# Performance work log

Measured on AMD Instinct MI355X. Metric: run time of the kernel, lower is better.

Reference implementation:

```python
import jax, jax.numpy as jnp
import numpy as np


def setup_inputs() -> dict:
    key = jax.random.key(0)
    k = jax.random.split(key, 5)
    B, Cin, Cout, H, W = 16, 32, 32, 256, 256
    m1, m2 = 16, 16
    scale = (1.0 / (Cin * Cout)) ** 0.5  # RandomUniform limit in original
    x = jax.random.normal(k[0], (B, Cin, H, W), dtype=jnp.float32)
    ws = {
        'w1_real': jax.random.uniform(k[1], (Cin, Cout, m1, m2), jnp.float32, -scale, scale),
        'w1_imag': jax.random.uniform(k[2], (Cin, Cout, m1, m2), jnp.float32, -scale, scale),
        'w2_real': jax.random.uniform(k[3], (Cin, Cout, m1, m2), jnp.float32, -scale, scale),
        'w2_imag': jax.random.uniform(k[4], (Cin, Cout, m1, m2), jnp.float32, -scale, scale),
    }
    return {'x': x, **ws}


def reference(x, w1_real, w1_imag, w2_real, w2_imag):
    B, Cin, H, W = x.shape
    Cout, m1, m2 = w1_real.shape[1], w1_real.shape[2], w1_real.shape[3]
    Wr = W // 2 + 1
    # full rFFT2 over (H, W); x_ft: [B, Cin, H, Wr] complex64
    x_ft = jnp.fft.rfft2(x, axes=(-2, -1))
    w1 = w1_real + 1j * w1_imag  # [Cin, Cout, m1, m2]
    w2 = w2_real + 1j * w2_imag
    top = jnp.einsum('bixy,ioxy->boxy', x_ft[:, :, :m1, :m2], w1)
    bottom = jnp.einsum('bixy,ioxy->boxy', x_ft[:, :, -m1:, :m2], w2)
    out_ft = jnp.zeros((B, Cout, H, Wr), dtype=x_ft.dtype)
    out_ft = out_ft.at[:, :, :m1, :m2].set(top)
    # original pads bottom block to start at row h_ft - m1 and ADDS the two padded tensors
    out_ft = out_ft.at[:, :, H - m1:, :m2].add(bottom)
    return jnp.fft.irfft2(out_ft, s=(H, W), axes=(-2, -1))
```

## Files before the change

### kernel.cpp

```cpp
#include <hip/hip_runtime.h>
#include <math.h>


#define TWO_PI_256 0.0245436926f

typedef short short8 __attribute__((ext_vector_type(8)));
typedef float f32x4  __attribute__((ext_vector_type(4)));

__device__ __forceinline__ ushort f2bf(float v) {
    unsigned u = __float_as_uint(v);
    u += 0x7FFFu + ((u >> 16) & 1u);
    return (ushort)(u >> 16);
}
__device__ __forceinline__ float bf2f(ushort h) {
    return __uint_as_float(((unsigned)h) << 16);
}

__global__ void init_frags(ushort* __restrict__ Fr) {
    const int s = blockIdx.x;
    const int lane = threadIdx.x;
    const int q = lane >> 4, n = lane & 15;
    for (int j = 0; j < 8; ++j) {
        float v = 0.f;
        int hl;
        if (s < 32) {
            int tn = s >> 4; hl = (s >> 3) & 1; int ch = s & 7;
            int w = ch * 32 + q * 8 + j, ky = n;
            float sn, cs; __sincosf((float)((w * ky) & 255) * TWO_PI_256, &sn, &cs);
            v = tn == 0 ? cs : -sn;
        } else if (s < 160) {
            int s2 = s - 32; int mt = s2 >> 5; hl = (s2 >> 4) & 1; int ch = s2 & 15;
            int m = mt * 16 + n, k = ch * 32 + q * 8 + j;
            int kxi = m >> 1, rx = m & 1, h = k >> 1, rt = k & 1;
            int r = kxi + (kxi >= 16 ? 224 : 0);
            float sn, cs; __sincosf((float)((r * h) & 255) * TWO_PI_256, &sn, &cs);
            v = (rx == 0) ? (rt == 0 ? cs : sn) : (rt == 0 ? -sn : cs);
        } else if (s < 288) {
            int s3 = s - 160; int mtG = s3 >> 2; hl = (s3 >> 1) & 1; int ch = s3 & 1;
            int m = mtG * 16 + n, k = ch * 32 + q * 8 + j;
            int h = m >> 1, rg = m & 1, kxi = k >> 1, ry = k & 1;
            int r = kxi + (kxi >= 16 ? 224 : 0);
            float sn, cs; __sincosf((float)((r * h) & 255) * TWO_PI_256, &sn, &cs);
            v = ((rg == 0) ? (ry == 0 ? cs : -sn) : (ry == 0 ? sn : cs)) * (1.0f / 65536.0f);
        } else {
            int s4 = s - 288; int nt = s4 >> 1; hl = s4 & 1;
            int k = q * 8 + j, w = nt * 16 + n;
            int ky = k >> 1, ri = k & 1;
            float sn, cs; __sincosf((float)((w * ky) & 255) * TWO_PI_256, &sn, &cs);
            v = (ky == 0) ? (ri ? 0.f : 1.f) : (ri ? -2.f * sn : 2.f * cs);
        }
        ushort hi = f2bf(v);
        Fr[s * 512 + lane * 8 + j] = hl == 0 ? hi : f2bf(v - bf2f(hi));
    }
}

__global__ __launch_bounds__(512) void f12_gemm(const float* __restrict__ x,
                                                const ushort* __restrict__ Fr,
                                                float* __restrict__ X) {
    __shared__ ushort LDS[16384];
    ushort* Ah = LDS;
    ushort* Al = LDS + 8192;
    ushort* Ts = LDS;

    const int t = threadIdx.x, bi = blockIdx.x;
    const int lane = t & 63, w = t >> 6;
    const int q = lane >> 4, n = lane & 15;
    const int srow = t >> 3, sw4 = t & 7;
    const float* xb = x + (size_t)bi * 65536;

    f32x4 acc[2][2];
    #pragma unroll
    for (int a = 0; a < 2; ++a)
        #pragma unroll
        for (int bb = 0; bb < 2; ++bb) acc[a][bb] = (f32x4){0.f, 0.f, 0.f, 0.f};

    for (int ch = 0; ch < 8; ++ch) {
        __syncthreads();
        #pragma unroll
        for (int m = 0; m < 4; ++m) {
            const int row = srow + 64 * m;
            float4 v = *(const float4*)(xb + (size_t)row * 256 + ch * 32 + sw4 * 4);
            ushort h0_ = f2bf(v.x), h1 = f2bf(v.y), h2 = f2bf(v.z), h3 = f2bf(v.w);
            *(ushort4*)&Ah[row * 32 + sw4 * 4] = make_ushort4(h0_, h1, h2, h3);
            *(ushort4*)&Al[row * 32 + sw4 * 4] = make_ushort4(f2bf(v.x - bf2f(h0_)), f2bf(v.y - bf2f(h1)),
                                                              f2bf(v.z - bf2f(h2)), f2bf(v.w - bf2f(h3)));
        }
        __syncthreads();

        short8 bh0 = *(const short8*)&Fr[(size_t)(0  + ch) * 512 + lane * 8];
        short8 bl0 = *(const short8*)&Fr[(size_t)(8  + ch) * 512 + lane * 8];
        short8 bh1 = *(const short8*)&Fr[(size_t)(16 + ch) * 512 + lane * 8];
        short8 bl1 = *(const short8*)&Fr[(size_t)(24 + ch) * 512 + lane * 8];

        #pragma unroll
        for (int mt = 0; mt < 2; ++mt) {
            const int row = w * 32 + mt * 16 + n;
            short8 ah = *(const short8*)&Ah[row * 32 + q * 8];
            short8 al = *(const short8*)&Al[row * 32 + q * 8];
            acc[mt][0] = __builtin_amdgcn_mfma_f32_16x16x32_bf16(al, bh0, acc[mt][0], 0, 0, 0);
            acc[mt][0] = __builtin_amdgcn_mfma_f32_16x16x32_bf16(ah, bl0, acc[mt][0], 0, 0, 0);
            acc[mt][0] = __builtin_amdgcn_mfma_f32_16x16x32_bf16(ah, bh0, acc[mt][0], 0, 0, 0);
            acc[mt][1] = __builtin_amdgcn_mfma_f32_16x16x32_bf16(al, bh1, acc[mt][1], 0, 0, 0);
            acc[mt][1] = __builtin_amdgcn_mfma_f32_16x16x32_bf16(ah, bl1, acc[mt][1], 0, 0, 0);
            acc[mt][1] = __builtin_amdgcn_mfma_f32_16x16x32_bf16(ah, bh1, acc[mt][1], 0, 0, 0);
        }
    }

    __syncthreads();
    #pragma unroll
    for (int mt = 0; mt < 2; ++mt) {
        ushort h8[8], l8[8];
        #pragma unroll
        for (int j = 0; j < 8; ++j) {
            float v = acc[mt][j & 1][j >> 1];
            h8[j] = f2bf(v);
            l8[j] = f2bf(v - bf2f(h8[j]));
        }
        const int c = w * 2 + mt;
        *(short8*)&Ts[c * 1024 + lane * 8]       = *(short8*)h8;
        *(short8*)&Ts[c * 1024 + 512 + lane * 8] = *(short8*)l8;
    }
    __syncthreads();

    if (w < 4) {
        const int mt2 = w;
        f32x4 a2 = (f32x4){0.f, 0.f, 0.f, 0.f};
        #pragma unroll
        for (int c2 = 0; c2 < 16; ++c2) {
            short8 bh = *(const short8*)&Ts[c2 * 1024 + lane * 8];
            short8 bl = *(const short8*)&Ts[c2 * 1024 + 512 + lane * 8];
            short8 ah = *(const short8*)&Fr[(size_t)(32 + mt2 * 32 + c2) * 512 + lane * 8];
            short8 al = *(const short8*)&Fr[(size_t)(32 + mt2 * 32 + 16 + c2) * 512 + lane * 8];
            a2 = __builtin_amdgcn_mfma_f32_16x16x32_bf16(al, bh, a2, 0, 0, 0);
            a2 = __builtin_amdgcn_mfma_f32_16x16x32_bf16(ah, bl, a2, 0, 0, 0);
            a2 = __builtin_amdgcn_mfma_f32_16x16x32_bf16(ah, bh, a2, 0, 0, 0);
        }
        #pragma unroll
        for (int r = 0; r < 4; ++r)
            X[(size_t)(mt2 * 16 + q * 4 + r) * 8192 + bi * 16 + n] = a2[r];
    }
}

__global__ __launch_bounds__(256) void mix(const float* __restrict__ X,
                                           const float* __restrict__ w1r_, const float* __restrict__ w1i_,
                                           const float* __restrict__ w2r_, const float* __restrict__ w2i_,
                                           float* __restrict__ Y) {
    int gid = blockIdx.x * 256 + threadIdx.x;
    int ky = gid & 15, kxi = (gid >> 4) & 31, o = (gid >> 9) & 31, b = gid >> 14;
    const float* wr = (kxi < 16) ? w1r_ : w2r_;
    const float* wi = (kxi < 16) ? w1i_ : w2i_;
    int xx = kxi & 15;
    const float* Xr = X + (size_t)(kxi * 2) * 8192 + b * 512 + ky;
    const float* Xi = Xr + 8192;
    const float* wrp = wr + (size_t)(o * 16 + xx) * 16 + ky;
    const float* wip = wi + (size_t)(o * 16 + xx) * 16 + ky;
    float yr = 0.f, yi = 0.f;
    #pragma unroll 8
    for (int i = 0; i < 32; ++i) {
        float xr = Xr[i * 16], xim = Xi[i * 16];
        float wre = wrp[(size_t)i * 8192], wim = wip[(size_t)i * 8192];
        yr = fmaf(xr, wre, fmaf(-xim, wim, yr));
        yi = fmaf(xr, wim, fmaf( xim, wre, yi));
    }
    size_t yb = (size_t)(kxi * 2) * 8192 + b * 512 + o * 16 + ky;
    Y[yb] = yr;
    Y[yb + 8192] = yi;
}

__global__ __launch_bounds__(512) void i12_gemm(const float* __restrict__ Yb,
                                                const ushort* __restrict__ Fr,
                                                float* __restrict__ out) {
    __shared__ ushort Bs[2048];
    __shared__ ushort As[16384];
    const int t = threadIdx.x, bo = blockIdx.x;
    const int lane = t & 63, w = t >> 6;
    const int q = lane >> 4, n = lane & 15;
    const int b = bo >> 5, o = bo & 31;

    if (t < 256) {
        const int k = t >> 2, e4 = t & 3;
        float4 v = *(const float4*)&Yb[(size_t)k * 8192 + b * 512 + o * 16 + e4 * 4];
        const int c = k >> 5, q2 = (k >> 3) & 3, j2 = k & 7;
        float vv[4] = {v.x, v.y, v.z, v.w};
        #pragma unroll
        for (int ee = 0; ee < 4; ++ee) {
            const int ky = e4 * 4 + ee;
            ushort hi = f2bf(vv[ee]);
            Bs[c * 1024 + (q2 * 16 + ky) * 8 + j2]       = hi;
            Bs[c * 1024 + 512 + (q2 * 16 + ky) * 8 + j2] = f2bf(vv[ee] - bf2f(hi));
        }
    }
    __syncthreads();

    f32x4 g[4];
    #pragma unroll
    for (int mi = 0; mi < 4; ++mi) g[mi] = (f32x4){0.f, 0.f, 0.f, 0.f};
    #pragma unroll
    for (int ch = 0; ch < 2; ++ch) {
        short8 bh = *(const short8*)&Bs[ch * 1024 + lane * 8];
        short8 bl = *(const short8*)&Bs[ch * 1024 + 512 + lane * 8];
        #pragma unroll
        for (int mi = 0; mi < 4; ++mi) {
            const int mtG = w * 4 + mi;
            short8 ah = *(const short8*)&Fr[(size_t)(160 + mtG * 4 + ch) * 512 + lane * 8];
            short8 al = *(const short8*)&Fr[(size_t)(160 + mtG * 4 + 2 + ch) * 512 + lane * 8];
            g[mi] = __builtin_amdgcn_mfma_f32_16x16x32_bf16(al, bh, g[mi], 0, 0, 0);
            g[mi] = __builtin_amdgcn_mfma_f32_16x16x32_bf16(ah, bl, g[mi], 0, 0, 0);
            g[mi] = __builtin_amdgcn_mfma_f32_16x16x32_bf16(ah, bh, g[mi], 0, 0, 0);
        }
    }

    #pragma unroll
    for (int mi = 0; mi < 4; ++mi)
        #pragma unroll
        for (int r = 0; r < 4; ++r) {
            const int m1 = (w * 4 + mi) * 16 + q * 4 + r;
            const int h = m1 >> 1, ri = m1 & 1;
            const int k2 = 2 * n + ri;
            const int ht = h >> 4, hr = h & 15;
            const int ad = ((k2 >> 3) * 16 + hr) * 8 + (k2 & 7);
            const float v = g[mi][r];
            const ushort hi = f2bf(v);
            As[ht * 1024 + ad]       = hi;
            As[ht * 1024 + 512 + ad] = f2bf(v - bf2f(hi));
        }
    __syncthreads();

    #pragma unroll
    for (int mi2 = 0; mi2 < 2; ++mi2) {
        const int ht2 = w * 2 + mi2;
        short8 ah = *(const short8*)&As[ht2 * 1024 + lane * 8];
        short8 al = *(const short8*)&As[ht2 * 1024 + 512 + lane * 8];
        f32x4 a3[16];
        #pragma unroll
        for (int nt = 0; nt < 16; ++nt) a3[nt] = (f32x4){0.f, 0.f, 0.f, 0.f};
        #pragma unroll
        for (int nt = 0; nt < 16; ++nt) {
            short8 bh = *(const short8*)&Fr[(size_t)(288 + nt * 2) * 512 + lane * 8];
            short8 bl = *(const short8*)&Fr[(size_t)(288 + nt * 2 + 1) * 512 + lane * 8];
            a3[nt] = __builtin_amdgcn_mfma_f32_16x16x32_bf16(al, bh, a3[nt], 0, 0, 0);
            a3[nt] = __builtin_amdgcn_mfma_f32_16x16x32_bf16(ah, bl, a3[nt], 0, 0, 0);
            a3[nt] = __builtin_amdgcn_mfma_f32_16x16x32_bf16(ah, bh, a3[nt], 0, 0, 0);
        }
        const size_t Rrow = (size_t)bo * 256 + ht2 * 16 + q * 4;
        #pragma unroll
        for (int nt = 0; nt < 16; ++nt)
            #pragma unroll
            for (int r = 0; r < 4; ++r)
                out[(Rrow + r) * 256 + nt * 16 + n] = a3[nt][r];
    }
}

extern "C" void kernel_launch(void* const* d_in, const int* in_sizes, int n_in,
                              void* d_out, int out_size, void* d_ws, size_t ws_size,
                              hipStream_t stream) {
    const float* x   = (const float*)d_in[0];
    const float* w1r = (const float*)d_in[1];
    const float* w1i = (const float*)d_in[2];
    const float* w2r = (const float*)d_in[3];
    const float* w2i = (const float*)d_in[4];
    float* out = (float*)d_out;

    ushort* Fr = (ushort*)d_ws;
    float*  X  = (float*)((char*)d_ws + (1u << 20));
    float*  Yb = X + (size_t)524288;

    init_frags<<<320,  64,  0, stream>>>(Fr);
    f12_gemm  <<<512,  512, 0, stream>>>(x, Fr, X);
    mix       <<<1024, 256, 0, stream>>>(X, w1r, w1i, w2r, w2i, Yb);
    i12_gemm  <<<512,  512, 0, stream>>>(Yb, Fr, out);
}
```

Measured before the change: 273.9 us.

## Fuse spectral mix into inverse GEMM and prefetch next input chunk in forward GEMM

The standalone mix kernel is removed. Its complex channel contraction now runs inside i12_gemm, where each of 512 threads computes one (kx, ky) output and writes the bf16 hi/lo split directly into shared memory. This drops one launch and the Yb round trip through global memory. The forward GEMM also loads the next 32-column chunk of x into registers right after the LDS barrier, overlapping that global load with the MFMA work, at the cost of extra registers.

```diff
diff --git a/kernel.cpp b/kernel.cpp
--- a/kernel.cpp
+++ b/kernel.cpp
@@ -74,18 +74,29 @@
         #pragma unroll
         for (int bb = 0; bb < 2; ++bb) acc[a][bb] = (f32x4){0.f, 0.f, 0.f, 0.f};
 
+    float4 vv[4];
+    #pragma unroll
+    for (int m = 0; m < 4; ++m)
+        vv[m] = *(const float4*)(xb + (size_t)(srow + 64 * m) * 256 + sw4 * 4);
+
     for (int ch = 0; ch < 8; ++ch) {
         __syncthreads();
         #pragma unroll
         for (int m = 0; m < 4; ++m) {
             const int row = srow + 64 * m;
-            float4 v = *(const float4*)(xb + (size_t)row * 256 + ch * 32 + sw4 * 4);
+            float4 v = vv[m];
             ushort h0_ = f2bf(v.x), h1 = f2bf(v.y), h2 = f2bf(v.z), h3 = f2bf(v.w);
             *(ushort4*)&Ah[row * 32 + sw4 * 4] = make_ushort4(h0_, h1, h2, h3);
             *(ushort4*)&Al[row * 32 + sw4 * 4] = make_ushort4(f2bf(v.x - bf2f(h0_)), f2bf(v.y - bf2f(h1)),
                                                               f2bf(v.z - bf2f(h2)), f2bf(v.w - bf2f(h3)));
         }
         __syncthreads();
+
+        if (ch < 7) {
+            #pragma unroll
+            for (int m = 0; m < 4; ++m)
+                vv[m] = *(const float4*)(xb + (size_t)(srow + 64 * m) * 256 + (ch + 1) * 32 + sw4 * 4);
+        }
 
         short8 bh0 = *(const short8*)&Fr[(size_t)(0  + ch) * 512 + lane * 8];
         short8 bl0 = *(const short8*)&Fr[(size_t)(8  + ch) * 512 + lane * 8];
@@ -141,33 +152,9 @@
     }
 }
 
-__global__ __launch_bounds__(256) void mix(const float* __restrict__ X,
-                                           const float* __restrict__ w1r_, const float* __restrict__ w1i_,
-                                           const float* __restrict__ w2r_, const float* __restrict__ w2i_,
-                                           float* __restrict__ Y) {
-    int gid = blockIdx.x * 256 + threadIdx.x;
-    int ky = gid & 15, kxi = (gid >> 4) & 31, o = (gid >> 9) & 31, b = gid >> 14;
-    const float* wr = (kxi < 16) ? w1r_ : w2r_;
-    const float* wi = (kxi < 16) ? w1i_ : w2i_;
-    int xx = kxi & 15;
-    const float* Xr = X + (size_t)(kxi * 2) * 8192 + b * 512 + ky;
-    const float* Xi = Xr + 8192;
-    const float* wrp = wr + (size_t)(o * 16 + xx) * 16 + ky;
-    const float* wip = wi + (size_t)(o * 16 + xx) * 16 + ky;
-    float yr = 0.f, yi = 0.f;
-    #pragma unroll 8
-    for (int i = 0; i < 32; ++i) {
-        float xr = Xr[i * 16], xim = Xi[i * 16];
-        float wre = wrp[(size_t)i * 8192], wim = wip[(size_t)i * 8192];
-        yr = fmaf(xr, wre, fmaf(-xim, wim, yr));
-        yi = fmaf(xr, wim, fmaf( xim, wre, yi));
-    }
-    size_t yb = (size_t)(kxi * 2) * 8192 + b * 512 + o * 16 + ky;
-    Y[yb] = yr;
-    Y[yb + 8192] = yi;
-}
-
-__global__ __launch_bounds__(512) void i12_gemm(const float* __restrict__ Yb,
+__global__ __launch_bounds__(512) void i12_gemm(const float* __restrict__ X,
+                                                const float* __restrict__ w1r_, const float* __restrict__ w1i_,
+                                                const float* __restrict__ w2r_, const float* __restrict__ w2i_,
                                                 const ushort* __restrict__ Fr,
                                                 float* __restrict__ out) {
     __shared__ ushort Bs[2048];
@@ -177,18 +164,31 @@
     const int q = lane >> 4, n = lane & 15;
     const int b = bo >> 5, o = bo & 31;
 
-    if (t < 256) {
-        const int k = t >> 2, e4 = t & 3;
-        float4 v = *(const float4*)&Yb[(size_t)k * 8192 + b * 512 + o * 16 + e4 * 4];
-        const int c = k >> 5, q2 = (k >> 3) & 3, j2 = k & 7;
-        float vv[4] = {v.x, v.y, v.z, v.w};
-        #pragma unroll
-        for (int ee = 0; ee < 4; ++ee) {
-            const int ky = e4 * 4 + ee;
-            ushort hi = f2bf(vv[ee]);
-            Bs[c * 1024 + (q2 * 16 + ky) * 8 + j2]       = hi;
-            Bs[c * 1024 + 512 + (q2 * 16 + ky) * 8 + j2] = f2bf(vv[ee] - bf2f(hi));
-        }
+    {
+        const int kxi = t >> 4, ky = t & 15;
+        const float* wr = (kxi < 16) ? w1r_ : w2r_;
+        const float* wi = (kxi < 16) ? w1i_ : w2i_;
+        const int xx = kxi & 15;
+        const float* Xr = X + (size_t)(kxi * 2) * 8192 + b * 512 + ky;
+        const float* Xi = Xr + 8192;
+        const float* wrp = wr + (size_t)(o * 16 + xx) * 16 + ky;
+        const float* wip = wi + (size_t)(o * 16 + xx) * 16 + ky;
+        float yr = 0.f, yi = 0.f;
+        #pragma unroll 8
+        for (int i = 0; i < 32; ++i) {
+            float xr = Xr[i * 16], xim = Xi[i * 16];
+            float wre = wrp[(size_t)i * 8192], wim = wip[(size_t)i * 8192];
+            yr = fmaf(xr, wre, fmaf(-xim, wim, yr));
+            yi = fmaf(xr, wim, fmaf( xim, wre, yi));
+        }
+        const int k0 = kxi * 2;
+        const int c = k0 >> 5, q2 = (k0 >> 3) & 3, j2 = k0 & 7;
+        ushort hr_ = f2bf(yr);
+        Bs[c * 1024 + (q2 * 16 + ky) * 8 + j2]           = hr_;
+        Bs[c * 1024 + 512 + (q2 * 16 + ky) * 8 + j2]     = f2bf(yr - bf2f(hr_));
+        ushort hi_ = f2bf(yi);
+        Bs[c * 1024 + (q2 * 16 + ky) * 8 + j2 + 1]       = hi_;
+        Bs[c * 1024 + 512 + (q2 * 16 + ky) * 8 + j2 + 1] = f2bf(yi - bf2f(hi_));
     }
     __syncthreads();
 
@@ -263,10 +263,8 @@
 
     ushort* Fr = (ushort*)d_ws;
     float*  X  = (float*)((char*)d_ws + (1u << 20));
-    float*  Yb = X + (size_t)524288;
 
     init_frags<<<320,  64,  0, stream>>>(Fr);
     f12_gemm  <<<512,  512, 0, stream>>>(x, Fr, X);
-    mix       <<<1024, 256, 0, stream>>>(X, w1r, w1i, w2r, w2i, Yb);
-    i12_gemm  <<<512,  512, 0, stream>>>(Yb, Fr, out);
-}
+    i12_gemm  <<<512,  512, 0, stream>>>(X, w1r, w1i, w2r, w2i, Fr, out);
+}
```

New measurement: 269.9 us. About the same (-1.5%).
